# Kernel optimization log

Measured on AMD Instinct MI355X. Metric: run time of the kernel, lower is better.

The kernel has to match this reference:

```python
import jax, jax.numpy as jnp
import numpy as np
from jax.scipy.special import logsumexp

DIM_N, DIM_E, DIM_U = 64, 128, 64
MID, A = 32, 16
N_PER, B = 12, 128  # 128 fully-connected graphs of 12 nodes


def _lin_params(k, fin, fout):
    k1, k2 = jax.random.split(k)
    lim = 1.0 / np.sqrt(fin)
    W = jax.random.uniform(k1, (fin, fout), minval=-lim, maxval=lim)
    b = jax.random.uniform(k2, (fout,), minval=-lim, maxval=lim)
    return W, b


def setup_inputs() -> dict:
    key = jax.random.key(0)
    ks = jax.random.split(key, 12)
    # fully connected directed graph (no self loops), per component
    s, d = np.meshgrid(np.arange(N_PER), np.arange(N_PER), indexing='ij')
    m = s != d
    s1, d1 = s[m].astype(np.int64), d[m].astype(np.int64)
    Epg = s1.size  # 132
    M = np.zeros((N_PER, N_PER), np.int64)
    M[s1, d1] = np.arange(Epg)
    rev1 = M[d1, s1]
    noff = (np.arange(B, dtype=np.int64) * N_PER)[:, None]
    eoff = (np.arange(B, dtype=np.int64) * Epg)[:, None]
    src = jnp.asarray((s1[None] + noff).reshape(-1))
    dst = jnp.asarray((d1[None] + noff).reshape(-1))
    idx_revs = jnp.asarray((rev1[None] + eoff).reshape(-1))
    E, Nt = B * Epg, B * N_PER
    edge_feats = jax.random.normal(ks[0], (E, DIM_E))
    node_feats = jax.random.normal(ks[1], (Nt, DIM_N))
    graph_feats = jax.random.normal(ks[2], (B, DIM_U))
    edge_feat_reflected = edge_feats[idx_revs]
    u = jax.random.uniform(ks[3], (E, 2), minval=1e-6, maxval=1.0)
    gumbel_noise = -jnp.log(-jnp.log(u))
    W_jf, b_jf = _lin_params(ks[4], DIM_E + DIM_U, A * MID)
    W_if, b_if = _lin_params(ks[5], DIM_N + DIM_U, A)
    W_ju, b_ju = _lin_params(ks[6], DIM_E + DIM_U, A * MID)
    W_iu, b_iu = _lin_params(ks[7], DIM_N + DIM_U, A)
    W_fl, b_fl = _lin_params(ks[8], DIM_E + DIM_U, MID)
    W_cls, b_cls = _lin_params(ks[9], MID, 2)
    return dict(edge_feats=edge_feats, node_feats=node_feats, graph_feats=graph_feats,
                edge_feat_reflected=edge_feat_reflected, src=src, dst=dst, idx_revs=idx_revs,
                gumbel_noise=gumbel_noise, W_jf=W_jf, b_jf=b_jf, W_if=W_if, b_if=b_if,
                W_ju=W_ju, b_ju=b_ju, W_iu=W_iu, b_iu=b_iu, W_fl=W_fl, b_fl=b_fl,
                W_cls=W_cls, b_cls=b_cls)


def reference(edge_feats, node_feats, graph_feats, edge_feat_reflected, src, dst, idx_revs,
              gumbel_noise, W_jf, b_jf, W_if, b_if, W_ju, b_ju, W_iu, b_iu,
              W_fl, b_fl, W_cls, b_cls):
    Bn = graph_feats.shape[0]
    Nt = node_feats.shape[0]
    E = edge_feats.shape[0]
    npg = Nt // Bn          # nodes per graph == number of BP iterations
    epg = E // Bn
    a = b_if.shape[0]       # num_acts
    mid = W_cls.shape[0]    # mid_pair

    # broadcast graph-level features to edges / nodes
    u_e = jnp.repeat(graph_feats, epg, axis=0)   # [E, du]
    u_n = jnp.repeat(graph_feats, npg, axis=0)   # [Nt, du]

    xe = jnp.concatenate([edge_feats, u_e], axis=-1)
    xer = jnp.concatenate([edge_feat_reflected, u_e], axis=-1)
    xn = jnp.concatenate([node_feats, u_n], axis=-1)

    indiv_factor = xn @ W_if + b_if      # [Nt, A]
    indiv_util = xn @ W_iu + b_iu        # [Nt, A]

    fc = (xe @ W_jf + b_jf).reshape(E, a, mid)
    fcr = (xer @ W_jf + b_jf).reshape(E, a, mid)
    factor_vals = jnp.einsum('eam,ebm->eab', fc, fcr)   # [E, A, A]
    uc = (xe @ W_ju + b_ju).reshape(E, a, mid)
    ucr = (xer @ W_ju + b_ju).reshape(E, a, mid)
    util_vals = jnp.einsum('eam,ebm->eab', uc, ucr)     # [E, A, A]

    # hard gumbel-softmax edge gating; noise shared with reverse edge
    flag_repr = (xe @ W_fl + b_fl) * (xer @ W_fl + b_fl)
    logits = flag_repr @ W_cls + b_cls                  # [E, 2]
    eid = jnp.arange(E)
    noise = gumbel_noise[jnp.minimum(eid, idx_revs)]
    y_soft = jax.nn.softmax(logits + noise, axis=-1)
    y_hard = jax.nn.one_hot(jnp.argmax(y_soft, axis=-1), 2, dtype=y_soft.dtype)
    flags = y_soft + jax.lax.stop_gradient(y_hard - y_soft)
    flag0 = flags[:, 0][:, None]                        # [E, 1]

    fvT = factor_vals.transpose(0, 2, 1)
    uvT = util_vals.transpose(0, 2, 1)
    if_src, if_dst = indiv_factor[src], indiv_factor[dst]
    iu_src, iu_dst = indiv_util[src], indiv_util[dst]

    def step(carry, _):
        mm_n, um_n, msg_e, rmsg_e, umsg_e, rumsg_e = carry
        agg = mm_n[src] - rmsg_e + if_src                      # [E, A]
        m = factor_vals + agg[:, None, :]                      # [E, A, A]
        m_sum = jax.nn.log_softmax(logsumexp(m, axis=-1), axis=-1)
        new_msg = m_sum * flag0
        agg_rev = mm_n[dst] - msg_e + if_dst
        m_rev = fvT + agg_rev[:, None, :]
        m_rev_sum = jax.nn.log_softmax(logsumexp(m_rev, axis=-1), axis=-1)
        new_rmsg = m_rev_sum * flag0
        util = um_n[src] - rumsg_e + iu_src
        new_umsg = ((util_vals + util[:, None, :]) * jax.nn.softmax(m, axis=-1)).sum(-1) * flag0
        rev_util = um_n[dst] - umsg_e + iu_dst
        new_rumsg = ((uvT + rev_util[:, None, :]) * jax.nn.softmax(m_rev, axis=-1)).sum(-1) * flag0
        new_mm_n = jax.ops.segment_sum(new_msg, dst, num_segments=Nt)
        new_um_n = jax.ops.segment_sum(new_umsg, dst, num_segments=Nt)
        return (new_mm_n, new_um_n, new_msg, new_rmsg, new_umsg, new_rumsg), None

    zn = jnp.zeros((Nt, a), edge_feats.dtype)
    ze = jnp.zeros((E, a), edge_feats.dtype)
    carry0 = (zn, zn, ze, ze, ze, ze)
    (mm_n, um_n, _, _, _, _), _ = jax.lax.scan(step, carry0, None, length=npg)

    node0 = jnp.arange(Bn) * npg
    return (um_n + indiv_util)[node0]   # [B, A]
```

## Files before the change

kernel.cpp:

```cpp
#include <hip/hip_runtime.h>
#include <hip/hip_bf16.h>

typedef unsigned short ushort_t;
typedef __bf16 bf16x8 __attribute__((ext_vector_type(8)));
typedef float f32x4 __attribute__((ext_vector_type(4)));

#define E_TOT 16896
#define NT    1536
#define BGR   128
#define NPG   12
#define EPG   132
#define KD    192
#define KDE   128
#define KD2   384
#define NJ    512
#define NCAN  8448

#if defined(__has_builtin)
#  if __has_builtin(__builtin_amdgcn_global_load_lds)
#    define HAS_GLL 1
#  else
#    define HAS_GLL 0
#  endif
#else
#  define HAS_GLL 0
#endif

#if HAS_GLL
__device__ __forceinline__ void gll16(const ushort_t* g, ushort_t* s) {
    __builtin_amdgcn_global_load_lds(
        (const __attribute__((address_space(1))) unsigned int*)g,
        (__attribute__((address_space(3))) unsigned int*)s, 16, 0, 0);
}
#endif

__device__ __forceinline__ float b2f(ushort_t u) {
    union { float f; unsigned int i; } c; c.i = ((unsigned int)u) << 16; return c.f;
}
__device__ __forceinline__ ushort_t f2b(float f) {
    union { float f; unsigned int i; } c; c.f = f;
    unsigned int i = c.i;
    unsigned int r = (i + 0x7FFFu + ((i >> 16) & 1u)) >> 16;
    return (ushort_t)r;
}
__device__ __forceinline__ int rev_local(int i) {
    int s = i / 11;
    int p = i - 11 * s;
    int d = p + (p >= s ? 1 : 0);
    return d * 11 + (s < d ? s : s - 1);
}

__global__ __launch_bounds__(256) void prep_kernel(
    const float* __restrict__ Wjf, const float* __restrict__ Wju,
    const float* __restrict__ ef,  const float* __restrict__ gf,
    const float* __restrict__ bjf, const float* __restrict__ bju,
    const float* __restrict__ nf,
    const float* __restrict__ Wif, const float* __restrict__ bif,
    const float* __restrict__ Wiu, const float* __restrict__ biu,
    ushort_t* __restrict__ WtJFs, ushort_t* __restrict__ WtJUs,
    ushort_t* __restrict__ XeS, float* __restrict__ CG,
    float* __restrict__ IFF, float* __restrict__ IUU)
{
    __shared__ union {
        float tile[64][65];
        struct { float Ws[128 * 32]; float xr[8][128]; } nd;
    } sm;
    int tid = threadIdx.x;
    unsigned bx = blockIdx.x;

    if (bx < 32u) {
        int mat = bx >> 4, t16 = bx & 15;
        int k0 = (t16 >> 3) * 64, n0 = (t16 & 7) * 64;
        const float* W = mat ? Wju : Wjf;
        ushort_t* Wt = mat ? WtJUs : WtJFs;
        int col = tid & 63, rowq = tid >> 6;
#pragma unroll
        for (int i = 0; i < 16; ++i) {
            int kk = i * 4 + rowq;
            sm.tile[kk][col] = W[(size_t)(k0 + kk) * NJ + n0 + col];
        }
        __syncthreads();
        int k = tid & 63;
#pragma unroll
        for (int i = 0; i < 16; ++i) {
            int nn = i * 4 + rowq;
            float wf = sm.tile[k][nn];
            ushort_t hf = f2b(wf);
            ushort_t lo = f2b(wf - b2f(hf));
            ushort_t* dst = Wt + (size_t)(n0 + nn) * KD2 + k0 + k;
            dst[0]   = hf;
            dst[128] = hf;
            dst[256] = lo;
        }
        return;
    }
    if (bx < 1088u) {
        int t = (int)(bx - 32u) * 256 + tid;
        int e = t >> 4, k8 = t & 15;
        const float* src = ef + (size_t)e * KDE + k8 * 8;
        float4 v0 = *(const float4*)(src);
        float4 v1 = *(const float4*)(src + 4);
        float x[8] = { v0.x, v0.y, v0.z, v0.w, v1.x, v1.y, v1.z, v1.w };
        union { ushort_t u[8]; uint4 v; } hi, lo;
#pragma unroll
        for (int i = 0; i < 8; ++i) {
            ushort_t h = f2b(x[i]);
            hi.u[i] = h;
            lo.u[i] = f2b(x[i] - b2f(h));
        }
        ushort_t* dst = XeS + (size_t)e * KD2 + k8 * 8;
        *(uint4*)(dst)       = hi.v;
        *(uint4*)(dst + 128) = lo.v;
        *(uint4*)(dst + 256) = hi.v;
        return;
    }
    if (bx < 1600u) {
        int cidx = (int)(bx - 1088u) * 256 + tid;
        int z = cidx >> 16;
        int rem = cidx & 65535;
        int g = rem >> 9, n = rem & 511;
        const float* W = z ? Wju : Wjf;
        float acc = (z ? bju : bjf)[n];
        const float* gr = gf + g * 64;
#pragma unroll 8
        for (int k = 0; k < 64; ++k)
            acc += gr[k] * W[(size_t)(KDE + k) * NJ + n];
        CG[cidx] = acc;
        return;
    }
    int n0 = (int)(bx - 1600u) * 8;
    for (int i = tid; i < 128 * 32; i += 256) {
        int k = i >> 5, j = i & 31;
        sm.nd.Ws[i] = (j < 16) ? Wif[k * 16 + j] : Wiu[k * 16 + (j - 16)];
    }
    for (int i = tid; i < 8 * 128; i += 256) {
        int slot = i >> 7, k = i & 127;
        int n = n0 + slot;
        sm.nd.xr[slot][k] = (k < 64) ? nf[(size_t)n * 64 + k]
                                     : gf[(n / NPG) * 64 + (k - 64)];
    }
    __syncthreads();
    int slot = tid >> 5, j = tid & 31;
    float acc = (j < 16) ? bif[j] : biu[j - 16];
#pragma unroll 8
    for (int k = 0; k < 128; ++k) acc += sm.nd.xr[slot][k] * sm.nd.Ws[k * 32 + j];
    int n = n0 + slot;
    if (j < 16) IFF[n * 16 + j] = acc;
    else        IUU[n * 16 + (j - 16)] = acc;
}

__global__ __launch_bounds__(256) void gemm_kernel(
    const ushort_t* __restrict__ X,
    const ushort_t* __restrict__ Wt0, const ushort_t* __restrict__ Wt1,
    const float* __restrict__ CG, float* __restrict__ Hbase)
{
    __shared__ ushort_t As[2][128][32];
    __shared__ ushort_t Bs[2][128][32];
    int z = blockIdx.z;
    const ushort_t* Wt = z ? Wt1 : Wt0;
    const float* cgz = CG + (size_t)z * 128 * NJ;
    float* H = Hbase + (size_t)z * E_TOT * NJ;

    int tid = threadIdx.x, lane = tid & 63, w = tid >> 6;
    int m0 = blockIdx.y * 128, n0 = blockIdx.x * 128;
    int wm = (w >> 1) * 64, wn = (w & 1) * 64;
    int r = lane & 15, q = lane >> 4;
    f32x4 acc[4][4] = {};

    int sr = w * 32 + (lane >> 2);
    int sc = (lane & 3) * 8;
    const ushort_t* xg0 = X  + (size_t)(m0 + sr)      * KD2 + sc;
    const ushort_t* xg1 = X  + (size_t)(m0 + sr + 16) * KD2 + sc;
    const ushort_t* wg0 = Wt + (size_t)(n0 + sr)      * KD2 + sc;
    const ushort_t* wg1 = Wt + (size_t)(n0 + sr + 16) * KD2 + sc;

#if HAS_GLL
    auto stage = [&](int p, int kk) {
        gll16(xg0 + kk, &As[p][w * 32][0]);
        gll16(xg1 + kk, &As[p][w * 32 + 16][0]);
        gll16(wg0 + kk, &Bs[p][w * 32][0]);
        gll16(wg1 + kk, &Bs[p][w * 32 + 16][0]);
    };
#else
    auto stage = [&](int p, int kk) {
        uint4 a0 = *(const uint4*)(xg0 + kk);
        uint4 a1 = *(const uint4*)(xg1 + kk);
        uint4 b0 = *(const uint4*)(wg0 + kk);
        uint4 b1 = *(const uint4*)(wg1 + kk);
        *(uint4*)&As[p][sr][sc]      = a0;
        *(uint4*)&As[p][sr + 16][sc] = a1;
        *(uint4*)&Bs[p][sr][sc]      = b0;
        *(uint4*)&Bs[p][sr + 16][sc] = b1;
    };
#endif

    stage(0, 0);
    int cur = 0;
    for (int kk = 0; kk < KD2; kk += 32) {
        __syncthreads();
        if (kk + 32 < KD2) stage(cur ^ 1, kk + 32);
        bf16x8 af[4], bf[4];
#pragma unroll
        for (int mi = 0; mi < 4; ++mi)
            af[mi] = *(const bf16x8*)&As[cur][wm + mi * 16 + r][q * 8];
#pragma unroll
        for (int ni = 0; ni < 4; ++ni)
            bf[ni] = *(const bf16x8*)&Bs[cur][wn + ni * 16 + r][q * 8];
#pragma unroll
        for (int mi = 0; mi < 4; ++mi)
#pragma unroll
            for (int ni = 0; ni < 4; ++ni)
                acc[mi][ni] = __builtin_amdgcn_mfma_f32_16x16x32_bf16(
                    af[mi], bf[ni], acc[mi][ni], 0, 0, 0);
        cur ^= 1;
    }
#pragma unroll
    for (int ni = 0; ni < 4; ++ni) {
        int col = n0 + wn + ni * 16 + r;
#pragma unroll
        for (int mi = 0; mi < 4; ++mi) {
            int rowb = m0 + wm + mi * 16 + q * 4;
            float* dst = H + (size_t)rowb * NJ + col;
#pragma unroll
            for (int rr = 0; rr < 4; ++rr) {
                int gg = (rowb + rr) / EPG;
                dst[(size_t)rr * NJ] = acc[mi][ni][rr] + cgz[(size_t)gg * NJ + col];
            }
        }
    }
}

__global__ __launch_bounds__(256) void pair_kernel(
    const float* __restrict__ Hbase, float* __restrict__ Obase)
{
    __shared__ float sA[4][16][36];
    __shared__ float sB[4][16][36];
    __shared__ float sC[4][16][20];
    const float* H = Hbase + (size_t)blockIdx.y * E_TOT * NJ;
    float* OutV = Obase + (size_t)blockIdx.y * E_TOT * 256;
    int tid = threadIdx.x, w = tid >> 6, lane = tid & 63;
    int c = blockIdx.x * 4 + w;
    int gg = c / 66, cl = c - gg * 66;
    int s = 0;
    while (cl >= 11 - s) { cl -= 11 - s; ++s; }
    int d = s + 1 + cl;
    int e  = gg * EPG + s * 11 + (d - 1);
    int re = gg * EPG + d * 11 + s;
    const float* hA = H + (size_t)e * NJ;
    const float* hB = H + (size_t)re * NJ;
    int a = lane >> 2, mseg = (lane & 3) * 8;
    float4 va0 = *(const float4*)(hA + a * 32 + mseg);
    float4 va1 = *(const float4*)(hA + a * 32 + mseg + 4);
    float4 vb0 = *(const float4*)(hB + a * 32 + mseg);
    float4 vb1 = *(const float4*)(hB + a * 32 + mseg + 4);
    *(float4*)&sA[w][a][mseg]     = va0;
    *(float4*)&sA[w][a][mseg + 4] = va1;
    *(float4*)&sB[w][a][mseg]     = vb0;
    *(float4*)&sB[w][a][mseg + 4] = vb1;
    __syncthreads();

    int b = lane & 15, a0 = (lane >> 4) * 4;
    float4 ac0 = {0,0,0,0}, ac1 = {0,0,0,0}, ac2 = {0,0,0,0}, ac3 = {0,0,0,0};
#pragma unroll
    for (int m4 = 0; m4 < 8; ++m4) {
        float4 vb = *(const float4*)&sB[w][b][m4 * 4];
        float4 x0 = *(const float4*)&sA[w][a0 + 0][m4 * 4];
        float4 x1 = *(const float4*)&sA[w][a0 + 1][m4 * 4];
        float4 x2 = *(const float4*)&sA[w][a0 + 2][m4 * 4];
        float4 x3 = *(const float4*)&sA[w][a0 + 3][m4 * 4];
        ac0.x += x0.x * vb.x; ac0.y += x0.y * vb.y; ac0.z += x0.z * vb.z; ac0.w += x0.w * vb.w;
        ac1.x += x1.x * vb.x; ac1.y += x1.y * vb.y; ac1.z += x1.z * vb.z; ac1.w += x1.w * vb.w;
        ac2.x += x2.x * vb.x; ac2.y += x2.y * vb.y; ac2.z += x2.z * vb.z; ac2.w += x2.w * vb.w;
        ac3.x += x3.x * vb.x; ac3.y += x3.y * vb.y; ac3.z += x3.z * vb.z; ac3.w += x3.w * vb.w;
    }
    float v0 = ac0.x + ac0.y + ac0.z + ac0.w;
    float v1 = ac1.x + ac1.y + ac1.z + ac1.w;
    float v2 = ac2.x + ac2.y + ac2.z + ac2.w;
    float v3 = ac3.x + ac3.y + ac3.z + ac3.w;
    float* oe = OutV + (size_t)e * 256;
    oe[(a0 + 0) * 16 + b] = v0;
    oe[(a0 + 1) * 16 + b] = v1;
    oe[(a0 + 2) * 16 + b] = v2;
    oe[(a0 + 3) * 16 + b] = v3;
    sC[w][b][a0 + 0] = v0;
    sC[w][b][a0 + 1] = v1;
    sC[w][b][a0 + 2] = v2;
    sC[w][b][a0 + 3] = v3;
    __syncthreads();
    int rr = lane >> 2, cc = (lane & 3) * 4;
    float4 t4 = { sC[w][rr][cc], sC[w][rr][cc + 1], sC[w][rr][cc + 2], sC[w][rr][cc + 3] };
    *(float4*)(OutV + (size_t)re * 256 + lane * 4) = t4;
}

__global__ __launch_bounds__(256) void hfl_kernel(
    const float* __restrict__ ef, const float* __restrict__ gf,
    const float* __restrict__ Wfl, const float* __restrict__ bfl,
    float* __restrict__ HFL)
{
    __shared__ float Ws[KD][32];
    __shared__ float xr[64][KD];
    int tid = threadIdx.x;
    int e0 = blockIdx.x * 64;
    for (int i = tid; i < KD * 32; i += 256) Ws[i >> 5][i & 31] = Wfl[i];
    for (int i4 = tid; i4 < 64 * 48; i4 += 256) {
        int slot = i4 / 48, kq = i4 - slot * 48;
        int e = e0 + slot;
        float4 v;
        if (kq < 32) v = *(const float4*)&ef[(size_t)e * 128 + kq * 4];
        else         v = *(const float4*)&gf[(e / EPG) * 64 + (kq - 32) * 4];
        *(float4*)&xr[slot][kq * 4] = v;
    }
    __syncthreads();
    int j = tid & 31, es = tid >> 5;
    float acc[8];
#pragma unroll
    for (int i = 0; i < 8; ++i) acc[i] = bfl[j];
    for (int k = 0; k < KD; k += 4) {
        float w0 = Ws[k][j], w1 = Ws[k + 1][j], w2 = Ws[k + 2][j], w3 = Ws[k + 3][j];
#pragma unroll
        for (int i = 0; i < 8; ++i) {
            float4 x4 = *(const float4*)&xr[es + 8 * i][k];
            acc[i] += x4.x * w0; acc[i] += x4.y * w1;
            acc[i] += x4.z * w2; acc[i] += x4.w * w3;
        }
    }
#pragma unroll
    for (int i = 0; i < 8; ++i)
        HFL[(size_t)(e0 + es + 8 * i) * 32 + j] = acc[i];
}

__global__ __launch_bounds__(704) void bp_kernel(
    const float* __restrict__ FV, const float* __restrict__ UV,
    const float* __restrict__ HFL, const float* __restrict__ Wcls,
    const float* __restrict__ bcls, const float* __restrict__ gum,
    const float* __restrict__ IFF, const float* __restrict__ IUU,
    float* __restrict__ out)
{
    int g = blockIdx.x, tid = threadIdx.x;
    __shared__ __align__(16) float fvs[EPG * 256];
    __shared__ __align__(16) float msg[EPG][16];
    __shared__ __align__(16) float umsg[EPG][16];
    __shared__ float Asum[NPG][16], Usum[NPG][16];
    __shared__ float iffs[NPG][16], iuus[NPG][16];
    __shared__ float fls[EPG];

    for (int i = tid; i < EPG * 16; i += 704) {
        (&msg[0][0])[i] = 0.f;
        (&umsg[0][0])[i] = 0.f;
    }
    if (tid < NPG * 16) {
        float fi = IFF[g * NPG * 16 + tid];
        float ui = IUU[g * NPG * 16 + tid];
        (&iffs[0][0])[tid] = fi; (&iuus[0][0])[tid] = ui;
        (&Asum[0][0])[tid] = fi; (&Usum[0][0])[tid] = ui;
    }
    if (tid < EPG) {
        int el = tid, rel = rev_local(el);
        int e = g * EPG + el, re = g * EPG + rel;
        float l0 = bcls[0], l1 = bcls[1];
        const float* ha = HFL + (size_t)e * 32;
        const float* hb = HFL + (size_t)re * 32;
#pragma unroll
        for (int j = 0; j < 32; ++j) {
            float pp = ha[j] * hb[j];
            l0 += pp * Wcls[j * 2 + 0];
            l1 += pp * Wcls[j * 2 + 1];
        }
        int mn = min(e, re);
        l0 += gum[(size_t)mn * 2 + 0];
        l1 += gum[(size_t)mn * 2 + 1];
        fls[el] = (l0 >= l1) ? 1.0f : 0.0f;
    }

    const float* fvg = FV + (size_t)g * EPG * 256;
    const float* uvg = UV + (size_t)g * EPG * 256;
    for (int t4 = tid; t4 < EPG * 64; t4 += 704) {
        float4 v = *(const float4*)(fvg + (size_t)t4 * 4);
        int e = t4 >> 6, rem = t4 & 63;
        int aa = rem >> 2, qq = rem & 3;
        int w = e * 256 + aa * 16 + ((qq ^ ((aa >> 1) & 3)) << 2);
        *(float4*)&fvs[w] = v;
    }

    int w44 = tid >> 4, a = tid & 15;
    int e0 = w44,      s0 = e0 / 11, r0 = rev_local(e0);
    int e1 = 44 + w44, s1 = e1 / 11, r1 = rev_local(e1);
    int e2 = 88 + w44, s2 = e2 / 11, r2 = rev_local(e2);

    int xr = (a >> 1) & 3;
    int sl0 = ((0 ^ xr) << 2), sl1 = ((1 ^ xr) << 2);
    int sl2 = ((2 ^ xr) << 2), sl3 = ((3 ^ xr) << 2);
    int fb0 = e0 * 256 + a * 16;
    int fb1 = e1 * 256 + a * 16;
    int fb2 = e2 * 256 + a * 16;

    const float* ur0 = uvg + (size_t)e0 * 256 + a * 16;
    const float* ur1 = uvg + (size_t)e1 * 256 + a * 16;
    const float* ur2 = uvg + (size_t)e2 * 256 + a * 16;

    __syncthreads();
    float fl0 = fls[e0], fl1 = fls[e1], fl2 = fls[e2];

    auto edge_core = [&](int s, int re, int fbase,
                         float4 u0, float4 u1, float4 u2, float4 u3,
                         float& lse_o, float& unv_o) {
        float4 f0 = *(const float4*)&fvs[fbase + sl0];
        float4 f1 = *(const float4*)&fvs[fbase + sl1];
        float4 f2 = *(const float4*)&fvs[fbase + sl2];
        float4 f3 = *(const float4*)&fvs[fbase + sl3];
        float m0, m1, m2, m3, m4, m5, m6, m7, m8, m9, m10, m11, m12, m13, m14, m15;
        {
            float4 av = *(const float4*)&Asum[s][0];
            float4 mv = *(const float4*)&msg[re][0];
            m0 = f0.x + (av.x - mv.x); m1 = f0.y + (av.y - mv.y);
            m2 = f0.z + (av.z - mv.z); m3 = f0.w + (av.w - mv.w);
        }
        {
            float4 av = *(const float4*)&Asum[s][4];
            float4 mv = *(const float4*)&msg[re][4];
            m4 = f1.x + (av.x - mv.x); m5 = f1.y + (av.y - mv.y);
            m6 = f1.z + (av.z - mv.z); m7 = f1.w + (av.w - mv.w);
        }
        {
            float4 av = *(const float4*)&Asum[s][8];
            float4 mv = *(const float4*)&msg[re][8];
            m8 = f2.x + (av.x - mv.x); m9 = f2.y + (av.y - mv.y);
            m10 = f2.z + (av.z - mv.z); m11 = f2.w + (av.w - mv.w);
        }
        {
            float4 av = *(const float4*)&Asum[s][12];
            float4 mv = *(const float4*)&msg[re][12];
            m12 = f3.x + (av.x - mv.x); m13 = f3.y + (av.y - mv.y);
            m14 = f3.z + (av.z - mv.z); m15 = f3.w + (av.w - mv.w);
        }
        float mx = m0;
        mx = fmaxf(mx, m1);  mx = fmaxf(mx, m2);  mx = fmaxf(mx, m3);
        mx = fmaxf(mx, m4);  mx = fmaxf(mx, m5);  mx = fmaxf(mx, m6);
        mx = fmaxf(mx, m7);  mx = fmaxf(mx, m8);  mx = fmaxf(mx, m9);
        mx = fmaxf(mx, m10); mx = fmaxf(mx, m11); mx = fmaxf(mx, m12);
        mx = fmaxf(mx, m13); mx = fmaxf(mx, m14); mx = fmaxf(mx, m15);
        float S = 0.f, num = 0.f;
        {
            float4 usv = *(const float4*)&Usum[s][0];
            float4 umv = *(const float4*)&umsg[re][0];
            float ev, tu;
            ev = __expf(m0 - mx); S += ev; tu = u0.x + (usv.x - umv.x); num += tu * ev;
            ev = __expf(m1 - mx); S += ev; tu = u0.y + (usv.y - umv.y); num += tu * ev;
            ev = __expf(m2 - mx); S += ev; tu = u0.z + (usv.z - umv.z); num += tu * ev;
            ev = __expf(m3 - mx); S += ev; tu = u0.w + (usv.w - umv.w); num += tu * ev;
        }
        {
            float4 usv = *(const float4*)&Usum[s][4];
            float4 umv = *(const float4*)&umsg[re][4];
            float ev, tu;
            ev = __expf(m4 - mx); S += ev; tu = u1.x + (usv.x - umv.x); num += tu * ev;
            ev = __expf(m5 - mx); S += ev; tu = u1.y + (usv.y - umv.y); num += tu * ev;
            ev = __expf(m6 - mx); S += ev; tu = u1.z + (usv.z - umv.z); num += tu * ev;
            ev = __expf(m7 - mx); S += ev; tu = u1.w + (usv.w - umv.w); num += tu * ev;
        }
        {
            float4 usv = *(const float4*)&Usum[s][8];
            float4 umv = *(const float4*)&umsg[re][8];
            float ev, tu;
            ev = __expf(m8 - mx);  S += ev; tu = u2.x + (usv.x - umv.x); num += tu * ev;
            ev = __expf(m9 - mx);  S += ev; tu = u2.y + (usv.y - umv.y); num += tu * ev;
            ev = __expf(m10 - mx); S += ev; tu = u2.z + (usv.z - umv.z); num += tu * ev;
            ev = __expf(m11 - mx); S += ev; tu = u2.w + (usv.w - umv.w); num += tu * ev;
        }
        {
            float4 usv = *(const float4*)&Usum[s][12];
            float4 umv = *(const float4*)&umsg[re][12];
            float ev, tu;
            ev = __expf(m12 - mx); S += ev; tu = u3.x + (usv.x - umv.x); num += tu * ev;
            ev = __expf(m13 - mx); S += ev; tu = u3.y + (usv.y - umv.y); num += tu * ev;
            ev = __expf(m14 - mx); S += ev; tu = u3.z + (usv.z - umv.z); num += tu * ev;
            ev = __expf(m15 - mx); S += ev; tu = u3.w + (usv.w - umv.w); num += tu * ev;
        }
        lse_o = mx + __logf(S);
        unv_o = num / S;
    };

    auto finish = [&](float lse, float unv, float fl, float& nm, float& nu) {
        float M2 = lse;
        M2 = fmaxf(M2, __shfl_xor(M2, 1));
        M2 = fmaxf(M2, __shfl_xor(M2, 2));
        M2 = fmaxf(M2, __shfl_xor(M2, 4));
        M2 = fmaxf(M2, __shfl_xor(M2, 8));
        float se = __expf(lse - M2);
        se += __shfl_xor(se, 1);
        se += __shfl_xor(se, 2);
        se += __shfl_xor(se, 4);
        se += __shfl_xor(se, 8);
        float LSE = M2 + __logf(se);
        nm = (lse - LSE) * fl;
        nu = unv * fl;
    };

    for (int it = 0; it < NPG - 1; ++it) {
        float4 u0q0 = *(const float4*)(ur0 + 0),  u0q1 = *(const float4*)(ur0 + 4);
        float4 u0q2 = *(const float4*)(ur0 + 8),  u0q3 = *(const float4*)(ur0 + 12);
        float4 u1q0 = *(const float4*)(ur1 + 0),  u1q1 = *(const float4*)(ur1 + 4);
        float4 u1q2 = *(const float4*)(ur1 + 8),  u1q3 = *(const float4*)(ur1 + 12);
        float4 u2q0 = *(const float4*)(ur2 + 0),  u2q1 = *(const float4*)(ur2 + 4);
        float4 u2q2 = *(const float4*)(ur2 + 8),  u2q3 = *(const float4*)(ur2 + 12);

        float lse0, unv0, lse1, unv1, lse2, unv2;
        edge_core(s0, r0, fb0, u0q0, u0q1, u0q2, u0q3, lse0, unv0);
        edge_core(s1, r1, fb1, u1q0, u1q1, u1q2, u1q3, lse1, unv1);
        edge_core(s2, r2, fb2, u2q0, u2q1, u2q2, u2q3, lse2, unv2);
        float nm0, nu0, nm1, nu1, nm2, nu2;
        finish(lse0, unv0, fl0, nm0, nu0);
        finish(lse1, unv1, fl1, nm1, nu1);
        finish(lse2, unv2, fl2, nm2, nu2);
        __syncthreads();
        msg[e0][a] = nm0; umsg[e0][a] = nu0;
        msg[e1][a] = nm1; umsg[e1][a] = nu1;
        msg[e2][a] = nm2; umsg[e2][a] = nu2;
        __syncthreads();
        if (tid < NPG * 16) {
            int n = tid >> 4, aa = tid & 15;
            float sm = 0.f, su = 0.f;
#pragma unroll
            for (int s = 0; s < NPG; ++s) {
                if (s == n) continue;
                int le = s * 11 + (n < s ? n : n - 1);
                sm += msg[le][aa];
                su += umsg[le][aa];
            }
            Asum[n][aa] = sm + iffs[n][aa];
            Usum[n][aa] = su + iuus[n][aa];
        }
        __syncthreads();
    }

    {
        float nu0 = 0.f, nu1 = 0.f, nu2 = 0.f;
        bool own = ((w44 % 11) == 0);
        if (own) {
            float lse, unv;
            if (e0 != 0) {
                float4 q0 = *(const float4*)(ur0 + 0), q1 = *(const float4*)(ur0 + 4);
                float4 q2 = *(const float4*)(ur0 + 8), q3 = *(const float4*)(ur0 + 12);
                edge_core(s0, r0, fb0, q0, q1, q2, q3, lse, unv);
                nu0 = unv * fl0;
            }
            {
                float4 q0 = *(const float4*)(ur1 + 0), q1 = *(const float4*)(ur1 + 4);
                float4 q2 = *(const float4*)(ur1 + 8), q3 = *(const float4*)(ur1 + 12);
                edge_core(s1, r1, fb1, q0, q1, q2, q3, lse, unv);
                nu1 = unv * fl1;
            }
            {
                float4 q0 = *(const float4*)(ur2 + 0), q1 = *(const float4*)(ur2 + 4);
                float4 q2 = *(const float4*)(ur2 + 8), q3 = *(const float4*)(ur2 + 12);
                edge_core(s2, r2, fb2, q0, q1, q2, q3, lse, unv);
                nu2 = unv * fl2;
            }
        }
        __syncthreads();
        if (own) {
            if (e0 != 0) umsg[e0][a] = nu0;
            umsg[e1][a] = nu1;
            umsg[e2][a] = nu2;
        }
        __syncthreads();
        if (tid < 16) {
            float su = 0.f;
#pragma unroll
            for (int s = 1; s < NPG; ++s) su += umsg[s * 11][tid];
            out[g * 16 + tid] = su + iuus[0][tid];
        }
    }
}

extern "C" void kernel_launch(void* const* d_in, const int* in_sizes, int n_in,
                              void* d_out, int out_size, void* d_ws, size_t ws_size,
                              hipStream_t stream) {
    const float* edge_feats  = (const float*)d_in[0];
    const float* node_feats  = (const float*)d_in[1];
    const float* graph_feats = (const float*)d_in[2];
    const float* gumbel      = (const float*)d_in[7];
    const float* W_jf        = (const float*)d_in[8];
    const float* b_jf        = (const float*)d_in[9];
    const float* W_if        = (const float*)d_in[10];
    const float* b_if        = (const float*)d_in[11];
    const float* W_ju        = (const float*)d_in[12];
    const float* b_ju        = (const float*)d_in[13];
    const float* W_iu        = (const float*)d_in[14];
    const float* b_iu        = (const float*)d_in[15];
    const float* W_fl        = (const float*)d_in[16];
    const float* b_fl        = (const float*)d_in[17];
    const float* W_cls       = (const float*)d_in[18];
    const float* b_cls       = (const float*)d_in[19];
    float* out = (float*)d_out;
    (void)in_sizes; (void)n_in; (void)out_size; (void)ws_size;

    size_t off = 0;
    char* base = (char*)d_ws;
    auto alloc = [&](size_t bytes) {
        void* p = base + off;
        off += (bytes + 255) & ~(size_t)255;
        return p;
    };
    ushort_t* XeS   = (ushort_t*)alloc((size_t)E_TOT * KD2 * 2);
    ushort_t* WtJFs = (ushort_t*)alloc((size_t)NJ * KD2 * 2);
    ushort_t* WtJUs = (ushort_t*)alloc((size_t)NJ * KD2 * 2);
    float*    CGp   = (float*)   alloc((size_t)2 * 128 * NJ * 4);
    float*    HFL   = (float*)   alloc((size_t)E_TOT * 32 * 4);
    float*    IFFp  = (float*)   alloc((size_t)NT * 16 * 4);
    float*    IUUp  = (float*)   alloc((size_t)NT * 16 * 4);
    float*    H2    = (float*)   alloc((size_t)E_TOT * NJ * 2 * 4);
    float*    FVUV  = (float*)   alloc((size_t)E_TOT * 512 * 4);
    float* FVv = FVUV;
    float* UVv = FVUV + (size_t)E_TOT * 256;

    const int prep_blocks = 32 + 1056 + 512 + 192;

    prep_kernel<<<prep_blocks, 256, 0, stream>>>(
        W_jf, W_ju, edge_feats, graph_feats, b_jf, b_ju, node_feats,
        W_if, b_if, W_iu, b_iu, WtJFs, WtJUs, XeS, CGp, IFFp, IUUp);
    hfl_kernel<<<E_TOT / 64, 256, 0, stream>>>(edge_feats, graph_feats, W_fl, b_fl, HFL);
    gemm_kernel<<<dim3(NJ / 128, E_TOT / 128, 2), 256, 0, stream>>>(
        XeS, WtJFs, WtJUs, CGp, H2);
    pair_kernel<<<dim3(NCAN / 4, 2), 256, 0, stream>>>(H2, FVUV);
    bp_kernel<<<BGR, 704, 0, stream>>>(FVv, UVv, HFL, W_cls, b_cls, gumbel,
                                       IFFp, IUUp, out);
}
```

Measured before the change: 234.4 us.

## Factor the message softmax into precomputed factor exponentials times per-lane aggregate exponentials

The per-edge factor values are turned into exp(fv - rowmax) once, before the belief-propagation loop, and written back to shared memory in place. Each iteration then computes only one exponential per lane for the incoming aggregate, after a 16-lane max reduction. That vector is shared through small LDS scratch arrays (gG/gU), and the logsumexp and utility sums become products of the stored exponentials. This removes the 16 exponentials and the 16-wide max per lane per edge per iteration, in exchange for extra shuffles and LDS round-trips. It also carries some risk of underflow or precision loss when factor and aggregate ranges are wide, which the S clamp only partly guards.

Measured after the change: 231.7 us. No clear change (-1.1%).

```diff
diff --git a/kernel.cpp b/kernel.cpp
--- a/kernel.cpp
+++ b/kernel.cpp
@@ -343,6 +343,8 @@
     __shared__ float Asum[NPG][16], Usum[NPG][16];
     __shared__ float iffs[NPG][16], iuus[NPG][16];
     __shared__ float fls[EPG];
+    __shared__ __align__(16) float gG[44][16];
+    __shared__ __align__(16) float gU[44][16];
 
     for (int i = tid; i < EPG * 16; i += 704) {
         (&msg[0][0])[i] = 0.f;
@@ -401,82 +403,79 @@
     __syncthreads();
     float fl0 = fls[e0], fl1 = fls[e1], fl2 = fls[e2];
 
-    auto edge_core = [&](int s, int re, int fbase,
+    auto xform = [&](int fbase) -> float {
+        float4 a0 = *(const float4*)&fvs[fbase + sl0];
+        float4 a1 = *(const float4*)&fvs[fbase + sl1];
+        float4 a2 = *(const float4*)&fvs[fbase + sl2];
+        float4 a3 = *(const float4*)&fvs[fbase + sl3];
+        float mx = fmaxf(fmaxf(fmaxf(a0.x, a0.y), fmaxf(a0.z, a0.w)),
+                         fmaxf(fmaxf(a1.x, a1.y), fmaxf(a1.z, a1.w)));
+        mx = fmaxf(mx, fmaxf(fmaxf(fmaxf(a2.x, a2.y), fmaxf(a2.z, a2.w)),
+                             fmaxf(fmaxf(a3.x, a3.y), fmaxf(a3.z, a3.w))));
+        a0.x = __expf(a0.x - mx); a0.y = __expf(a0.y - mx);
+        a0.z = __expf(a0.z - mx); a0.w = __expf(a0.w - mx);
+        a1.x = __expf(a1.x - mx); a1.y = __expf(a1.y - mx);
+        a1.z = __expf(a1.z - mx); a1.w = __expf(a1.w - mx);
+        a2.x = __expf(a2.x - mx); a2.y = __expf(a2.y - mx);
+        a2.z = __expf(a2.z - mx); a2.w = __expf(a2.w - mx);
+        a3.x = __expf(a3.x - mx); a3.y = __expf(a3.y - mx);
+        a3.z = __expf(a3.z - mx); a3.w = __expf(a3.w - mx);
+        *(float4*)&fvs[fbase + sl0] = a0;
+        *(float4*)&fvs[fbase + sl1] = a1;
+        *(float4*)&fvs[fbase + sl2] = a2;
+        *(float4*)&fvs[fbase + sl3] = a3;
+        return mx;
+    };
+    float fvm0 = xform(fb0);
+    float fvm1 = xform(fb1);
+    float fvm2 = xform(fb2);
+
+    auto edge_core = [&](int s, int re, int fbase, float fvm,
                          float4 u0, float4 u1, float4 u2, float4 u3,
                          float& lse_o, float& unv_o) {
-        float4 f0 = *(const float4*)&fvs[fbase + sl0];
-        float4 f1 = *(const float4*)&fvs[fbase + sl1];
-        float4 f2 = *(const float4*)&fvs[fbase + sl2];
-        float4 f3 = *(const float4*)&fvs[fbase + sl3];
-        float m0, m1, m2, m3, m4, m5, m6, m7, m8, m9, m10, m11, m12, m13, m14, m15;
-        {
-            float4 av = *(const float4*)&Asum[s][0];
-            float4 mv = *(const float4*)&msg[re][0];
-            m0 = f0.x + (av.x - mv.x); m1 = f0.y + (av.y - mv.y);
-            m2 = f0.z + (av.z - mv.z); m3 = f0.w + (av.w - mv.w);
-        }
-        {
-            float4 av = *(const float4*)&Asum[s][4];
-            float4 mv = *(const float4*)&msg[re][4];
-            m4 = f1.x + (av.x - mv.x); m5 = f1.y + (av.y - mv.y);
-            m6 = f1.z + (av.z - mv.z); m7 = f1.w + (av.w - mv.w);
-        }
-        {
-            float4 av = *(const float4*)&Asum[s][8];
-            float4 mv = *(const float4*)&msg[re][8];
-            m8 = f2.x + (av.x - mv.x); m9 = f2.y + (av.y - mv.y);
-            m10 = f2.z + (av.z - mv.z); m11 = f2.w + (av.w - mv.w);
-        }
-        {
-            float4 av = *(const float4*)&Asum[s][12];
-            float4 mv = *(const float4*)&msg[re][12];
-            m12 = f3.x + (av.x - mv.x); m13 = f3.y + (av.y - mv.y);
-            m14 = f3.z + (av.z - mv.z); m15 = f3.w + (av.w - mv.w);
-        }
-        float mx = m0;
-        mx = fmaxf(mx, m1);  mx = fmaxf(mx, m2);  mx = fmaxf(mx, m3);
-        mx = fmaxf(mx, m4);  mx = fmaxf(mx, m5);  mx = fmaxf(mx, m6);
-        mx = fmaxf(mx, m7);  mx = fmaxf(mx, m8);  mx = fmaxf(mx, m9);
-        mx = fmaxf(mx, m10); mx = fmaxf(mx, m11); mx = fmaxf(mx, m12);
-        mx = fmaxf(mx, m13); mx = fmaxf(mx, m14); mx = fmaxf(mx, m15);
-        float S = 0.f, num = 0.f;
-        {
-            float4 usv = *(const float4*)&Usum[s][0];
-            float4 umv = *(const float4*)&umsg[re][0];
-            float ev, tu;
-            ev = __expf(m0 - mx); S += ev; tu = u0.x + (usv.x - umv.x); num += tu * ev;
-            ev = __expf(m1 - mx); S += ev; tu = u0.y + (usv.y - umv.y); num += tu * ev;
-            ev = __expf(m2 - mx); S += ev; tu = u0.z + (usv.z - umv.z); num += tu * ev;
-            ev = __expf(m3 - mx); S += ev; tu = u0.w + (usv.w - umv.w); num += tu * ev;
-        }
-        {
-            float4 usv = *(const float4*)&Usum[s][4];
-            float4 umv = *(const float4*)&umsg[re][4];
-            float ev, tu;
-            ev = __expf(m4 - mx); S += ev; tu = u1.x + (usv.x - umv.x); num += tu * ev;
-            ev = __expf(m5 - mx); S += ev; tu = u1.y + (usv.y - umv.y); num += tu * ev;
-            ev = __expf(m6 - mx); S += ev; tu = u1.z + (usv.z - umv.z); num += tu * ev;
-            ev = __expf(m7 - mx); S += ev; tu = u1.w + (usv.w - umv.w); num += tu * ev;
-        }
-        {
-            float4 usv = *(const float4*)&Usum[s][8];
-            float4 umv = *(const float4*)&umsg[re][8];
-            float ev, tu;
-            ev = __expf(m8 - mx);  S += ev; tu = u2.x + (usv.x - umv.x); num += tu * ev;
-            ev = __expf(m9 - mx);  S += ev; tu = u2.y + (usv.y - umv.y); num += tu * ev;
-            ev = __expf(m10 - mx); S += ev; tu = u2.z + (usv.z - umv.z); num += tu * ev;
-            ev = __expf(m11 - mx); S += ev; tu = u2.w + (usv.w - umv.w); num += tu * ev;
-        }
-        {
-            float4 usv = *(const float4*)&Usum[s][12];
-            float4 umv = *(const float4*)&umsg[re][12];
-            float ev, tu;
-            ev = __expf(m12 - mx); S += ev; tu = u3.x + (usv.x - umv.x); num += tu * ev;
-            ev = __expf(m13 - mx); S += ev; tu = u3.y + (usv.y - umv.y); num += tu * ev;
-            ev = __expf(m14 - mx); S += ev; tu = u3.z + (usv.z - umv.z); num += tu * ev;
-            ev = __expf(m15 - mx); S += ev; tu = u3.w + (usv.w - umv.w); num += tu * ev;
-        }
-        lse_o = mx + __logf(S);
+        float aggA  = Asum[s][a] - msg[re][a];
+        float uaggA = Usum[s][a] - umsg[re][a];
+        float amx = aggA;
+        amx = fmaxf(amx, __shfl_xor(amx, 1));
+        amx = fmaxf(amx, __shfl_xor(amx, 2));
+        amx = fmaxf(amx, __shfl_xor(amx, 4));
+        amx = fmaxf(amx, __shfl_xor(amx, 8));
+        gG[w44][a] = __expf(aggA - amx);
+        gU[w44][a] = uaggA;
+        float4 G0 = *(const float4*)&gG[w44][0];
+        float4 G1 = *(const float4*)&gG[w44][4];
+        float4 G2 = *(const float4*)&gG[w44][8];
+        float4 G3 = *(const float4*)&gG[w44][12];
+        float4 U0 = *(const float4*)&gU[w44][0];
+        float4 U1 = *(const float4*)&gU[w44][4];
+        float4 U2 = *(const float4*)&gU[w44][8];
+        float4 U3 = *(const float4*)&gU[w44][12];
+        float4 E0 = *(const float4*)&fvs[fbase + sl0];
+        float4 E1 = *(const float4*)&fvs[fbase + sl1];
+        float4 E2 = *(const float4*)&fvs[fbase + sl2];
+        float4 E3 = *(const float4*)&fvs[fbase + sl3];
+        float p0  = E0.x * G0.x, p1  = E0.y * G0.y;
+        float p2  = E0.z * G0.z, p3  = E0.w * G0.w;
+        float p4  = E1.x * G1.x, p5  = E1.y * G1.y;
+        float p6  = E1.z * G1.z, p7  = E1.w * G1.w;
+        float p8  = E2.x * G2.x, p9  = E2.y * G2.y;
+        float p10 = E2.z * G2.z, p11 = E2.w * G2.w;
+        float p12 = E3.x * G3.x, p13 = E3.y * G3.y;
+        float p14 = E3.z * G3.z, p15 = E3.w * G3.w;
+        float S = (((p0 + p1) + (p2 + p3)) + ((p4 + p5) + (p6 + p7)))
+                + (((p8 + p9) + (p10 + p11)) + ((p12 + p13) + (p14 + p15)));
+        float n0  = (u0.x + U0.x) * p0,  n1  = (u0.y + U0.y) * p1;
+        float n2  = (u0.z + U0.z) * p2,  n3  = (u0.w + U0.w) * p3;
+        float n4  = (u1.x + U1.x) * p4,  n5  = (u1.y + U1.y) * p5;
+        float n6  = (u1.z + U1.z) * p6,  n7  = (u1.w + U1.w) * p7;
+        float n8  = (u2.x + U2.x) * p8,  n9  = (u2.y + U2.y) * p9;
+        float n10 = (u2.z + U2.z) * p10, n11 = (u2.w + U2.w) * p11;
+        float n12 = (u3.x + U3.x) * p12, n13 = (u3.y + U3.y) * p13;
+        float n14 = (u3.z + U3.z) * p14, n15 = (u3.w + U3.w) * p15;
+        float num = (((n0 + n1) + (n2 + n3)) + ((n4 + n5) + (n6 + n7)))
+                  + (((n8 + n9) + (n10 + n11)) + ((n12 + n13) + (n14 + n15)));
+        S = fmaxf(S, 1e-37f);
+        lse_o = (fvm + amx) + __logf(S);
         unv_o = num / S;
     };
 
@@ -505,9 +504,9 @@
         float4 u2q2 = *(const float4*)(ur2 + 8),  u2q3 = *(const float4*)(ur2 + 12);
 
         float lse0, unv0, lse1, unv1, lse2, unv2;
-        edge_core(s0, r0, fb0, u0q0, u0q1, u0q2, u0q3, lse0, unv0);
-        edge_core(s1, r1, fb1, u1q0, u1q1, u1q2, u1q3, lse1, unv1);
-        edge_core(s2, r2, fb2, u2q0, u2q1, u2q2, u2q3, lse2, unv2);
+        edge_core(s0, r0, fb0, fvm0, u0q0, u0q1, u0q2, u0q3, lse0, unv0);
+        edge_core(s1, r1, fb1, fvm1, u1q0, u1q1, u1q2, u1q3, lse1, unv1);
+        edge_core(s2, r2, fb2, fvm2, u2q0, u2q1, u2q2, u2q3, lse2, unv2);
         float nm0, nu0, nm1, nu1, nm2, nu2;
         finish(lse0, unv0, fl0, nm0, nu0);
         finish(lse1, unv1, fl1, nm1, nu1);
@@ -541,19 +540,19 @@
             if (e0 != 0) {
                 float4 q0 = *(const float4*)(ur0 + 0), q1 = *(const float4*)(ur0 + 4);
                 float4 q2 = *(const float4*)(ur0 + 8), q3 = *(const float4*)(ur0 + 12);
-                edge_core(s0, r0, fb0, q0, q1, q2, q3, lse, unv);
+                edge_core(s0, r0, fb0, fvm0, q0, q1, q2, q3, lse, unv);
                 nu0 = unv * fl0;
             }
             {
                 float4 q0 = *(const float4*)(ur1 + 0), q1 = *(const float4*)(ur1 + 4);
                 float4 q2 = *(const float4*)(ur1 + 8), q3 = *(const float4*)(ur1 + 12);
-                edge_core(s1, r1, fb1, q0, q1, q2, q3, lse, unv);
+                edge_core(s1, r1, fb1, fvm1, q0, q1, q2, q3, lse, unv);
                 nu1 = unv * fl1;
             }
             {
                 float4 q0 = *(const float4*)(ur2 + 0), q1 = *(const float4*)(ur2 + 4);
                 float4 q2 = *(const float4*)(ur2 + 8), q3 = *(const float4*)(ur2 + 12);
-                edge_core(s2, r2, fb2, q0, q1, q2, q3, lse, unv);
+                edge_core(s2, r2, fb2, fvm2, q0, q1, q2, q3, lse, unv);
                 nu2 = unv * fl2;
             }
         }
```
